# Kernel optimization log

Hardware: AMD Instinct MI355X
Metric: run time of the kernel (lower is better)

## Reference

```python
import jax, jax.numpy as jnp
import numpy as np

B, C, D, K = 16, 512, 256, 32

def setup_inputs() -> dict:
    key = jax.random.key(0)
    ks = jax.random.split(key, 6)
    s = 1.0 / np.sqrt(D)
    return {
        "h": jax.random.normal(ks[0], (B, C, D), dtype=jnp.float32),
        "topk_idx": jax.random.randint(ks[1], (B, C, K), 0, C, dtype=jnp.int64),
        "topk_scores": jax.random.normal(ks[2], (B, C, K), dtype=jnp.float32),
        "vW": jax.random.normal(ks[3], (D, D), dtype=jnp.float32) * s,
        "vb": jnp.zeros((D,), dtype=jnp.float32),
        "oW": jax.random.normal(ks[4], (D, D), dtype=jnp.float32) * s,
        "ob": jnp.zeros((D,), dtype=jnp.float32),
        "gW": jax.random.normal(ks[5], (2 * D, D), dtype=jnp.float32) * s,
        "gb": jnp.zeros((D,), dtype=jnp.float32),
    }

def reference(h, topk_idx, topk_scores, vW, vb, oW, ob, gW, gb):
    # Gather K neighbor features per (batch, channel): [B, C, K, D]
    b_idx = jnp.arange(h.shape[0])[:, None, None]
    neigh = h[b_idx, topk_idx]                         # [B,C,K,D]
    attn = jax.nn.softmax(topk_scores, axis=-1)        # [B,C,K]
    neigh = jnp.einsum('bckd,de->bcke', neigh, vW) + vb  # v_proj
    agg = jnp.einsum('bck,bckd->bcd', attn, neigh)      # weighted sum
    gate = jax.nn.sigmoid(jnp.concatenate([h, agg], axis=-1) @ gW + gb)
    delta = gate * (agg @ oW + ob)
    return delta
```

## Files before the change

kernel.cpp:

```cpp
#include <hip/hip_runtime.h>
#include <hip/hip_bf16.h>
#include <cstdint>
#include <cstddef>

using short8  = __attribute__((ext_vector_type(8))) short;
using short4v = __attribute__((ext_vector_type(4))) short;
using f32x4   = __attribute__((ext_vector_type(4))) float;

constexpr int NB = 16, NC = 512, ND = 256, NK = 32;
constexpr int ROWS = 32;
constexpr int NROW = NB * NC;
constexpr int NBLK = NROW / ROWS;
constexpr int NTHR = 512;

constexpr int OFF_SW = 32768;
constexpr int OFF_HB = 49152;

constexpr int PVW = 0;
constexpr int POW = 65536;
constexpr int PGW = 131072;
constexpr int PHB = 262144;
constexpr size_t WS_NEED = (size_t)(PHB + NB * 131072) * 2;

static __device__ __forceinline__ unsigned short f2bf(float f) {
    __hip_bfloat16 b = __float2bfloat16(f);
    return *reinterpret_cast<unsigned short*>(&b);
}
static __device__ __forceinline__ short4v f2bf4(float4 v) {
    short4v r;
    r[0] = (short)f2bf(v.x); r[1] = (short)f2bf(v.y);
    r[2] = (short)f2bf(v.z); r[3] = (short)f2bf(v.w);
    return r;
}

__global__ __launch_bounds__(256)
void stk_pack_all(const float* __restrict__ vW, const float* __restrict__ oW,
                  const float* __restrict__ gW, const float* __restrict__ h,
                  unsigned short* __restrict__ ws)
{
    const int blk = blockIdx.x;
    if (blk < 128) {
        const int tid  = blk * 256 + threadIdx.x;
        const int lane = tid & 63;
        const int fl   = tid >> 6;
        const float* src; int nt, ks;
        if (fl < 128)      { src = vW; nt = fl >> 3;         ks = fl & 7;          }
        else if (fl < 256) { src = oW; nt = (fl - 128) >> 3; ks = (fl - 128) & 7;  }
        else               { src = gW; nt = (fl - 256) >> 4; ks = (fl - 256) & 15; }
        const int col = nt * 16 + (lane & 15);
        const int k0  = ks * 32 + (lane >> 4) * 8;
        short8 v;
        #pragma unroll
        for (int j = 0; j < 8; ++j)
            v[j] = (short)f2bf(src[(size_t)(k0 + j) * ND + col]);
        *reinterpret_cast<short8*>(&ws[(size_t)tid * 8]) = v;
    } else {
        const int tid  = (blk - 128) * 256 + threadIdx.x;
        const int lane = tid & 63;
        const int fs   = tid >> 6;
        const int b    = fs >> 8;
        const int ks   = (fs >> 4) & 15;
        const int nt   = fs & 15;
        const float* src = h + (size_t)b * NC * ND;
        const int col = nt * 16 + (lane & 15);
        const int k0  = ks * 32 + (lane >> 4) * 8;
        short8 v;
        #pragma unroll
        for (int j = 0; j < 8; ++j)
            v[j] = (short)f2bf(src[(size_t)(k0 + j) * ND + col]);
        *reinterpret_cast<short8*>(&ws[(size_t)PHB + (size_t)tid * 8]) = v;
    }
}

__global__ __launch_bounds__(512, 4)
void stk_main(const float* __restrict__ h,
              const int*   __restrict__ topk_idx,
              const float* __restrict__ topk_scores,
              const float* __restrict__ vb, const float* __restrict__ ob,
              const float* __restrict__ gb,
              const unsigned short* __restrict__ wsb,
              float* __restrict__ out)
{
    __shared__ __align__(16) char smem[65536];
    float (*s_P)[512] = reinterpret_cast<float(*)[512]>(smem);

    const int t   = threadIdx.x;
    const int bid = (int)blockIdx.x;
    const int swz = ((bid & 7) << 5) + (bid >> 3);
    const int m0  = swz * ROWS;
    const int batch = m0 >> 9;

    const int hr = t >> 4;
    const int hc = (t & 15) * 16;
    short4v hreg[4];
    {
        const float* hrow = h + (size_t)(m0 + hr) * ND + hc;
        #pragma unroll
        for (int u = 0; u < 4; ++u)
            hreg[u] = f2bf4(*reinterpret_cast<const float4*>(hrow + 4 * u));
    }

    {
        float4* p4 = reinterpret_cast<float4*>(smem);
        #pragma unroll
        for (int i = 0; i < 8; ++i)
            p4[t + 512 * i] = float4{0.f, 0.f, 0.f, 0.f};
    }

    const int k  = t & 31;
    const int r0 = t >> 5;
    float att[2]; int id[2];
    #pragma unroll
    for (int half = 0; half < 2; ++half) {
        const int r = r0 + (half << 4);
        const size_t off = (size_t)(m0 + r) * NK + k;
        const float s = topk_scores[off];
        id[half] = topk_idx[off];
        float m = s;
        #pragma unroll
        for (int msk = 16; msk >= 1; msk >>= 1)
            m = fmaxf(m, __shfl_xor(m, msk));
        const float p = __expf(s - m);
        float Z = p;
        #pragma unroll
        for (int msk = 16; msk >= 1; msk >>= 1)
            Z += __shfl_xor(Z, msk);
        att[half] = p / Z;
    }
    __syncthreads();

    atomicAdd(&s_P[r0][id[0]],      att[0]);
    atomicAdd(&s_P[r0 + 16][id[1]], att[1]);
    __syncthreads();

    {
        const int pr  = t >> 4;
        const int pc4 = (t & 15) * 4;
        float4 pch[8];
        #pragma unroll
        for (int u = 0; u < 8; ++u)
            pch[u] = *reinterpret_cast<const float4*>(&s_P[pr][pc4 + 64 * u]);
        __syncthreads();

        const int xr = (pr & 7) << 4;
        #pragma unroll
        for (int u = 0; u < 8; ++u)
            *reinterpret_cast<short4v*>(
                smem + pr * 1024 + (((pc4 + 64 * u) * 2) ^ xr)) = f2bf4(pch[u]);
        const int xh = (hr & 7) << 4;
        #pragma unroll
        for (int u = 0; u < 4; ++u)
            *reinterpret_cast<short4v*>(
                smem + OFF_HB + hr * 512 + (((hc + 4 * u) * 2) ^ xh)) = hreg[u];
    }
    __syncthreads();

    const int lane = t & 63, w = t >> 6;
    const int n0 = 2 * w, lr = lane & 15, lg = lane >> 4;
    const int xa = (lr & 7) << 4;

    {
        f32x4 acc[2][2] = {{f32x4{0,0,0,0}, f32x4{0,0,0,0}},
                           {f32x4{0,0,0,0}, f32x4{0,0,0,0}}};
        const unsigned short* hf = wsb + (size_t)PHB + (size_t)batch * 131072;
        #pragma unroll
        for (int ks = 0; ks < 16; ++ks) {
            const int cb = (ks * 32 + lg * 8) * 2;
            short8 a[2];
            a[0] = *reinterpret_cast<const short8*>(smem + lr * 1024 + (cb ^ xa));
            a[1] = *reinterpret_cast<const short8*>(smem + (16 + lr) * 1024 + (cb ^ xa));
            #pragma unroll
            for (int n = 0; n < 2; ++n) {
                const short8 b = *reinterpret_cast<const short8*>(
                    &hf[((size_t)(ks * 16 + n0 + n) * 64 + lane) * 8]);
                acc[0][n] = __builtin_amdgcn_mfma_f32_16x16x32_bf16(a[0], b, acc[0][n], 0, 0, 0);
                acc[1][n] = __builtin_amdgcn_mfma_f32_16x16x32_bf16(a[1], b, acc[1][n], 0, 0, 0);
            }
        }
        #pragma unroll
        for (int m = 0; m < 2; ++m)
            #pragma unroll
            for (int n = 0; n < 2; ++n) {
                const int col = (n0 + n) * 16 + lr;
                #pragma unroll
                for (int q = 0; q < 4; ++q) {
                    const int row = m * 16 + 4 * lg + q;
                    *reinterpret_cast<unsigned short*>(
                        smem + OFF_SW + row * 512 + ((col * 2) ^ ((row & 7) << 4))) =
                        f2bf(acc[m][n][q]);
                }
            }
    }
    __syncthreads();

    {
        f32x4 acc[2][2];
        #pragma unroll
        for (int n = 0; n < 2; ++n) {
            const float bv = vb[(n0 + n) * 16 + lr];
            acc[0][n] = f32x4{bv, bv, bv, bv};
            acc[1][n] = f32x4{bv, bv, bv, bv};
        }
        #pragma unroll
        for (int ks = 0; ks < 8; ++ks) {
            const int cb = (ks * 32 + lg * 8) * 2;
            short8 a[2];
            a[0] = *reinterpret_cast<const short8*>(smem + OFF_SW + lr * 512 + (cb ^ xa));
            a[1] = *reinterpret_cast<const short8*>(smem + OFF_SW + (16 + lr) * 512 + (cb ^ xa));
            #pragma unroll
            for (int n = 0; n < 2; ++n) {
                const short8 b = *reinterpret_cast<const short8*>(
                    &wsb[(size_t)(PVW + (((n0 + n) * 8 + ks) * 64 + lane) * 8)]);
                acc[0][n] = __builtin_amdgcn_mfma_f32_16x16x32_bf16(a[0], b, acc[0][n], 0, 0, 0);
                acc[1][n] = __builtin_amdgcn_mfma_f32_16x16x32_bf16(a[1], b, acc[1][n], 0, 0, 0);
            }
        }
        #pragma unroll
        for (int m = 0; m < 2; ++m)
            #pragma unroll
            for (int n = 0; n < 2; ++n) {
                const int col = (n0 + n) * 16 + lr;
                #pragma unroll
                for (int q = 0; q < 4; ++q) {
                    const int row = m * 16 + 4 * lg + q;
                    *reinterpret_cast<unsigned short*>(
                        smem + row * 512 + ((col * 2) ^ ((row & 7) << 4))) =
                        f2bf(acc[m][n][q]);
                }
            }
    }
    __syncthreads();

    {
        f32x4 ao[2][2], ag[2][2];
        #pragma unroll
        for (int n = 0; n < 2; ++n) {
            const float bo = ob[(n0 + n) * 16 + lr];
            const float bg = gb[(n0 + n) * 16 + lr];
            ao[0][n] = f32x4{bo, bo, bo, bo}; ao[1][n] = ao[0][n];
            ag[0][n] = f32x4{bg, bg, bg, bg}; ag[1][n] = ag[0][n];
        }
        #pragma unroll
        for (int ks = 0; ks < 8; ++ks) {
            const int cb = (ks * 32 + lg * 8) * 2;
            short8 aa[2], ah[2];
            aa[0] = *reinterpret_cast<const short8*>(smem + lr * 512 + (cb ^ xa));
            aa[1] = *reinterpret_cast<const short8*>(smem + (16 + lr) * 512 + (cb ^ xa));
            ah[0] = *reinterpret_cast<const short8*>(smem + OFF_HB + lr * 512 + (cb ^ xa));
            ah[1] = *reinterpret_cast<const short8*>(smem + OFF_HB + (16 + lr) * 512 + (cb ^ xa));
            #pragma unroll
            for (int n = 0; n < 2; ++n) {
                const int nt = n0 + n;
                const short8 b_o  = *reinterpret_cast<const short8*>(
                    &wsb[(size_t)(POW + ((nt * 8 + ks) * 64 + lane) * 8)]);
                const short8 b_g1 = *reinterpret_cast<const short8*>(
                    &wsb[(size_t)(PGW + ((nt * 16 + ks) * 64 + lane) * 8)]);
                const short8 b_g2 = *reinterpret_cast<const short8*>(
                    &wsb[(size_t)(PGW + ((nt * 16 + ks + 8) * 64 + lane) * 8)]);
                #pragma unroll
                for (int m = 0; m < 2; ++m) {
                    ao[m][n] = __builtin_amdgcn_mfma_f32_16x16x32_bf16(aa[m], b_o,  ao[m][n], 0, 0, 0);
                    ag[m][n] = __builtin_amdgcn_mfma_f32_16x16x32_bf16(ah[m], b_g1, ag[m][n], 0, 0, 0);
                    ag[m][n] = __builtin_amdgcn_mfma_f32_16x16x32_bf16(aa[m], b_g2, ag[m][n], 0, 0, 0);
                }
            }
        }
        #pragma unroll
        for (int m = 0; m < 2; ++m)
            #pragma unroll
            for (int n = 0; n < 2; ++n) {
                const int col = (n0 + n) * 16 + lr;
                #pragma unroll
                for (int q = 0; q < 4; ++q) {
                    const int row = m0 + m * 16 + 4 * lg + q;
                    const float g = 1.f / (1.f + __expf(-ag[m][n][q]));
                    out[(size_t)row * ND + col] = g * ao[m][n][q];
                }
            }
    }
}

__global__ __launch_bounds__(512, 2)
void stk_fused(const float* __restrict__ h,
               const int*   __restrict__ topk_idx,
               const float* __restrict__ topk_scores,
               const float* __restrict__ vW, const float* __restrict__ vb,
               const float* __restrict__ oW, const float* __restrict__ ob,
               const float* __restrict__ gW, const float* __restrict__ gb,
               float* __restrict__ out)
{
    __shared__ float s_attn[32][NK];
    __shared__ int   s_idx [32][NK];
    __shared__ float s_wsum[32][ND];
    __shared__ float s_h   [32][ND];
    __shared__ float s_agg [32][ND];

    const int t  = threadIdx.x;
    const int m0 = blockIdx.x * 32;
    const size_t hb = (size_t)(m0 >> 9) * NC * ND;

    {
        const int k  = t & 31;
        const int r0 = t >> 5;
        #pragma unroll
        for (int half = 0; half < 2; ++half) {
            const int r = r0 + (half << 4);
            const size_t off = (size_t)(m0 + r) * NK + k;
            const float s = topk_scores[off];
            const int  id = topk_idx[off];
            float m = s;
            #pragma unroll
            for (int msk = 16; msk >= 1; msk >>= 1) m = fmaxf(m, __shfl_xor(m, msk));
            const float p = __expf(s - m);
            float Z = p;
            #pragma unroll
            for (int msk = 16; msk >= 1; msk >>= 1) Z += __shfl_xor(Z, msk);
            s_attn[r][k] = p / Z;
            s_idx [r][k] = id;
        }
    }
    __syncthreads();

    const int d  = t & 127;
    const int rb = (t >> 7) * 8;

    #pragma unroll
    for (int i = 0; i < 8; ++i) {
        const int r = rb + i;
        const size_t ro = (size_t)(m0 + r) * ND;
        s_h[r][d]       = h[ro + d];
        s_h[r][d + 128] = h[ro + d + 128];
    }
    #pragma unroll 1
    for (int i = 0; i < 8; ++i) {
        const int r = rb + i;
        float a0 = 0.f, a1 = 0.f;
        #pragma unroll 8
        for (int k = 0; k < NK; ++k) {
            const float w  = s_attn[r][k];
            const size_t nb = hb + (size_t)s_idx[r][k] * ND;
            a0 = fmaf(w, h[nb + d],       a0);
            a1 = fmaf(w, h[nb + d + 128], a1);
        }
        s_wsum[r][d]       = a0;
        s_wsum[r][d + 128] = a1;
    }
    __syncthreads();

    float agg0[8], agg1[8];
    {
        const float b0 = vb[d], b1 = vb[d + 128];
        #pragma unroll
        for (int i = 0; i < 8; ++i) { agg0[i] = b0; agg1[i] = b1; }
        for (int e0 = 0; e0 < ND; e0 += 4) {
            float w0[4], w1[4];
            #pragma unroll
            for (int j = 0; j < 4; ++j) {
                w0[j] = vW[(size_t)(e0 + j) * ND + d];
                w1[j] = vW[(size_t)(e0 + j) * ND + d + 128];
            }
            #pragma unroll
            for (int i = 0; i < 8; ++i) {
                const float4 a = *reinterpret_cast<const float4*>(&s_wsum[rb + i][e0]);
                agg0[i] = fmaf(a.x, w0[0], agg0[i]); agg1[i] = fmaf(a.x, w1[0], agg1[i]);
                agg0[i] = fmaf(a.y, w0[1], agg0[i]); agg1[i] = fmaf(a.y, w1[1], agg1[i]);
                agg0[i] = fmaf(a.z, w0[2], agg0[i]); agg1[i] = fmaf(a.z, w1[2], agg1[i]);
                agg0[i] = fmaf(a.w, w0[3], agg0[i]); agg1[i] = fmaf(a.w, w1[3], agg1[i]);
            }
        }
        #pragma unroll
        for (int i = 0; i < 8; ++i) {
            s_agg[rb + i][d]       = agg0[i];
            s_agg[rb + i][d + 128] = agg1[i];
        }
    }
    __syncthreads();

    float o0[8], o1[8], g0[8], g1[8];
    {
        const float obb0 = ob[d], obb1 = ob[d + 128];
        const float gbb0 = gb[d], gbb1 = gb[d + 128];
        #pragma unroll
        for (int i = 0; i < 8; ++i) { o0[i]=obb0; o1[i]=obb1; g0[i]=gbb0; g1[i]=gbb1; }
        for (int e0 = 0; e0 < ND; e0 += 4) {
            float ow0[4], ow1[4], gh0[4], gh1[4], ga0[4], ga1[4];
            #pragma unroll
            for (int j = 0; j < 4; ++j) {
                const size_t er = (size_t)(e0 + j) * ND;
                ow0[j] = oW[er + d];                    ow1[j] = oW[er + d + 128];
                gh0[j] = gW[er + d];                    gh1[j] = gW[er + d + 128];
                ga0[j] = gW[er + (size_t)ND * ND + d];  ga1[j] = gW[er + (size_t)ND * ND + d + 128];
            }
            #pragma unroll
            for (int i = 0; i < 8; ++i) {
                const float4 a  = *reinterpret_cast<const float4*>(&s_agg[rb + i][e0]);
                const float4 hh = *reinterpret_cast<const float4*>(&s_h  [rb + i][e0]);
                o0[i] = fmaf(a.x, ow0[0], o0[i]); o0[i] = fmaf(a.y, ow0[1], o0[i]);
                o0[i] = fmaf(a.z, ow0[2], o0[i]); o0[i] = fmaf(a.w, ow0[3], o0[i]);
                o1[i] = fmaf(a.x, ow1[0], o1[i]); o1[i] = fmaf(a.y, ow1[1], o1[i]);
                o1[i] = fmaf(a.z, ow1[2], o1[i]); o1[i] = fmaf(a.w, ow1[3], o1[i]);
                g0[i] = fmaf(hh.x, gh0[0], g0[i]); g0[i] = fmaf(hh.y, gh0[1], g0[i]);
                g0[i] = fmaf(hh.z, gh0[2], g0[i]); g0[i] = fmaf(hh.w, gh0[3], g0[i]);
                g1[i] = fmaf(hh.x, gh1[0], g1[i]); g1[i] = fmaf(hh.y, gh1[1], g1[i]);
                g1[i] = fmaf(hh.z, gh1[2], g1[i]); g1[i] = fmaf(hh.w, gh1[3], g1[i]);
                g0[i] = fmaf(a.x, ga0[0], g0[i]); g0[i] = fmaf(a.y, ga0[1], g0[i]);
                g0[i] = fmaf(a.z, ga0[2], g0[i]); g0[i] = fmaf(a.w, ga0[3], g0[i]);
                g1[i] = fmaf(a.x, ga1[0], g1[i]); g1[i] = fmaf(a.y, ga1[1], g1[i]);
                g1[i] = fmaf(a.z, ga1[2], g1[i]); g1[i] = fmaf(a.w, ga1[3], g1[i]);
            }
        }
    }
    #pragma unroll
    for (int i = 0; i < 8; ++i) {
        const size_t ro = (size_t)(m0 + rb + i) * ND;
        const float sg0 = 1.f / (1.f + __expf(-g0[i]));
        const float sg1 = 1.f / (1.f + __expf(-g1[i]));
        out[ro + d]       = sg0 * o0[i];
        out[ro + d + 128] = sg1 * o1[i];
    }
}

extern "C" void kernel_launch(void* const* d_in, const int* in_sizes, int n_in,
                              void* d_out, int out_size, void* d_ws, size_t ws_size,
                              hipStream_t stream) {
    const float* h   = (const float*)d_in[0];
    const int*   idx = (const int*)  d_in[1];
    const float* sc  = (const float*)d_in[2];
    const float* vW  = (const float*)d_in[3];
    const float* vb  = (const float*)d_in[4];
    const float* oW  = (const float*)d_in[5];
    const float* ob  = (const float*)d_in[6];
    const float* gW  = (const float*)d_in[7];
    const float* gb  = (const float*)d_in[8];
    float* out = (float*)d_out;

    if (ws_size >= WS_NEED) {
        unsigned short* wsb = (unsigned short*)d_ws;
        stk_pack_all<<<1152, 256, 0, stream>>>(vW, oW, gW, h, wsb);
        stk_main    <<<NBLK, NTHR, 0, stream>>>(h, idx, sc, vb, ob, gb, wsb, out);
    } else {
        stk_fused<<<256, 512, 0, stream>>>(h, idx, sc, vW, vb, oW, ob, gW, gb, out);
    }
}
```

Baseline: 28.70 us.

## Fuse weight/h packing into main kernel via cooperative grid sync

Merges the separate bf16 packing kernel into the main kernel. Every block now packs a slice of h and the weights, then waits on a cooperative-groups grid barrier before the MFMA stages. The goal is to drop one kernel launch and its inter-kernel gap. The cost is a grid-wide sync, which needs all 256 blocks of 512 threads to be co-resident and adds barrier latency. Each block's h-pack slice is chosen by bid&7, apparently so the packed data lands on the same XCD that later reads it.

Result: slower. 64.29 us (+124.0%).

```diff
diff --git a/kernel.cpp b/kernel.cpp
--- a/kernel.cpp
+++ b/kernel.cpp
@@ -1,7 +1,10 @@
 #include <hip/hip_runtime.h>
+#include <hip/hip_cooperative_groups.h>
 #include <hip/hip_bf16.h>
 #include <cstdint>
 #include <cstddef>
+
+namespace cg = cooperative_groups;
 
 using short8  = __attribute__((ext_vector_type(8))) short;
 using short4v = __attribute__((ext_vector_type(4))) short;
@@ -33,53 +36,51 @@
     return r;
 }
 
-__global__ __launch_bounds__(256)
-void stk_pack_all(const float* __restrict__ vW, const float* __restrict__ oW,
-                  const float* __restrict__ gW, const float* __restrict__ h,
-                  unsigned short* __restrict__ ws)
+static __device__ __forceinline__ void pack_weight_unit(
+    int u, const float* __restrict__ vW, const float* __restrict__ oW,
+    const float* __restrict__ gW, unsigned short* __restrict__ ws)
 {
-    const int blk = blockIdx.x;
-    if (blk < 128) {
-        const int tid  = blk * 256 + threadIdx.x;
-        const int lane = tid & 63;
-        const int fl   = tid >> 6;
-        const float* src; int nt, ks;
-        if (fl < 128)      { src = vW; nt = fl >> 3;         ks = fl & 7;          }
-        else if (fl < 256) { src = oW; nt = (fl - 128) >> 3; ks = (fl - 128) & 7;  }
-        else               { src = gW; nt = (fl - 256) >> 4; ks = (fl - 256) & 15; }
-        const int col = nt * 16 + (lane & 15);
-        const int k0  = ks * 32 + (lane >> 4) * 8;
-        short8 v;
-        #pragma unroll
-        for (int j = 0; j < 8; ++j)
-            v[j] = (short)f2bf(src[(size_t)(k0 + j) * ND + col]);
-        *reinterpret_cast<short8*>(&ws[(size_t)tid * 8]) = v;
-    } else {
-        const int tid  = (blk - 128) * 256 + threadIdx.x;
-        const int lane = tid & 63;
-        const int fs   = tid >> 6;
-        const int b    = fs >> 8;
-        const int ks   = (fs >> 4) & 15;
-        const int nt   = fs & 15;
-        const float* src = h + (size_t)b * NC * ND;
-        const int col = nt * 16 + (lane & 15);
-        const int k0  = ks * 32 + (lane >> 4) * 8;
-        short8 v;
-        #pragma unroll
-        for (int j = 0; j < 8; ++j)
-            v[j] = (short)f2bf(src[(size_t)(k0 + j) * ND + col]);
-        *reinterpret_cast<short8*>(&ws[(size_t)PHB + (size_t)tid * 8]) = v;
-    }
+    const int lane = u & 63;
+    const int fl   = u >> 6;
+    const float* src; int nt, ks;
+    if (fl < 128)      { src = vW; nt = fl >> 3;         ks = fl & 7;          }
+    else if (fl < 256) { src = oW; nt = (fl - 128) >> 3; ks = (fl - 128) & 7;  }
+    else               { src = gW; nt = (fl - 256) >> 4; ks = (fl - 256) & 15; }
+    const int col = nt * 16 + (lane & 15);
+    const int k0  = ks * 32 + (lane >> 4) * 8;
+    short8 v;
+    #pragma unroll
+    for (int j = 0; j < 8; ++j)
+        v[j] = (short)f2bf(src[(size_t)(k0 + j) * ND + col]);
+    *reinterpret_cast<short8*>(&ws[(size_t)u * 8]) = v;
+}
+static __device__ __forceinline__ void pack_h_unit(
+    int hu, const float* __restrict__ h, unsigned short* __restrict__ ws)
+{
+    const int lane = hu & 63;
+    const int fs   = hu >> 6;
+    const int b    = fs >> 8;
+    const int ks   = (fs >> 4) & 15;
+    const int nt   = fs & 15;
+    const float* src = h + (size_t)b * NC * ND;
+    const int col = nt * 16 + (lane & 15);
+    const int k0  = ks * 32 + (lane >> 4) * 8;
+    short8 v;
+    #pragma unroll
+    for (int j = 0; j < 8; ++j)
+        v[j] = (short)f2bf(src[(size_t)(k0 + j) * ND + col]);
+    *reinterpret_cast<short8*>(&ws[(size_t)PHB + (size_t)hu * 8]) = v;
 }
 
 __global__ __launch_bounds__(512, 4)
-void stk_main(const float* __restrict__ h,
-              const int*   __restrict__ topk_idx,
-              const float* __restrict__ topk_scores,
-              const float* __restrict__ vb, const float* __restrict__ ob,
-              const float* __restrict__ gb,
-              const unsigned short* __restrict__ wsb,
-              float* __restrict__ out)
+void stk_one(const float* __restrict__ h,
+             const int*   __restrict__ topk_idx,
+             const float* __restrict__ topk_scores,
+             const float* __restrict__ vW, const float* __restrict__ vb,
+             const float* __restrict__ oW, const float* __restrict__ ob,
+             const float* __restrict__ gW, const float* __restrict__ gb,
+             unsigned short* __restrict__ wsb,
+             float* __restrict__ out)
 {
     __shared__ __align__(16) char smem[65536];
     float (*s_P)[512] = reinterpret_cast<float(*)[512]>(smem);
@@ -90,6 +91,15 @@
     const int m0  = swz * ROWS;
     const int batch = m0 >> 9;
 
+    {
+        const int xcd = bid & 7;
+        const int lt  = (bid >> 3) * 512 + t;
+        pack_h_unit(xcd * 32768 + lt,          h, wsb);
+        pack_h_unit(xcd * 32768 + lt + 16384,  h, wsb);
+        const int g = bid * 512 + t;
+        if (g < 32768) pack_weight_unit(g, vW, oW, gW, wsb);
+    }
+
     const int hr = t >> 4;
     const int hc = (t & 15) * 16;
     short4v hreg[4];
@@ -99,14 +109,12 @@
         for (int u = 0; u < 4; ++u)
             hreg[u] = f2bf4(*reinterpret_cast<const float4*>(hrow + 4 * u));
     }
-
     {
         float4* p4 = reinterpret_cast<float4*>(smem);
         #pragma unroll
         for (int i = 0; i < 8; ++i)
             p4[t + 512 * i] = float4{0.f, 0.f, 0.f, 0.f};
     }
-
     const int k  = t & 31;
     const int r0 = t >> 5;
     float att[2]; int id[2];
@@ -153,7 +161,8 @@
             *reinterpret_cast<short4v*>(
                 smem + OFF_HB + hr * 512 + (((hc + 4 * u) * 2) ^ xh)) = hreg[u];
     }
-    __syncthreads();
+
+    cg::this_grid().sync();
 
     const int lane = t & 63, w = t >> 6;
     const int n0 = 2 * w, lr = lane & 15, lg = lane >> 4;
@@ -436,8 +445,13 @@
 
     if (ws_size >= WS_NEED) {
         unsigned short* wsb = (unsigned short*)d_ws;
-        stk_pack_all<<<1152, 256, 0, stream>>>(vW, oW, gW, h, wsb);
-        stk_main    <<<NBLK, NTHR, 0, stream>>>(h, idx, sc, vb, ob, gb, wsb, out);
+        void* kargs[] = {
+            (void*)&h, (void*)&idx, (void*)&sc,
+            (void*)&vW, (void*)&vb, (void*)&oW, (void*)&ob,
+            (void*)&gW, (void*)&gb, (void*)&wsb, (void*)&out
+        };
+        hipLaunchCooperativeKernel((void*)stk_one, dim3(NBLK), dim3(NTHR),
+                                   kargs, 0, stream);
     } else {
         stk_fused<<<256, 512, 0, stream>>>(h, idx, sc, vW, vb, oW, ob, gW, gb, out);
     }
```
